# Performance work log

Hardware: AMD Instinct MI355X
Metric: run time of the kernel (lower is better)

Reference implementation:

```python
import jax, jax.numpy as jnp
import numpy as np

FP8_MAX = 448.0  # torch.finfo(float8_e4m3fn).max


def per_tensor_quantize(t):
    amax = jnp.max(jnp.abs(t))
    scale = jnp.maximum(amax, 1e-12) / FP8_MAX
    q = jnp.clip(t / scale, -FP8_MAX, FP8_MAX)
    return q, scale.astype(jnp.float32)


def fp8_cast(t):
    # round-to-fp8-e4m3 and back (value-faithful to .to(float8_e4m3fn)),
    # straight-through so it is also usable under vjp
    rounded = t.astype(jnp.float8_e4m3fn).astype(t.dtype)
    return t + jax.lax.stop_gradient(rounded - t)


def setup_inputs() -> dict:
    key = jax.random.key(0)
    k1, k2, k3 = jax.random.split(key, 3)
    B, S, D_IN, D_OUT = 4, 2048, 4096, 4096
    x = jax.random.normal(k1, (B, S, D_IN), dtype=jnp.float32)
    # build a pre-quantized weight exactly like the repo would: quantize a float weight
    w = jax.random.normal(k2, (D_OUT, D_IN), dtype=jnp.float32) * 0.02
    qweight, weight_scale = per_tensor_quantize(w)
    bias = jax.random.normal(k3, (D_OUT,), dtype=jnp.float32) * 0.01
    return {"x": x, "qweight": qweight, "weight_scale": weight_scale, "bias": bias}


def reference(x, qweight, weight_scale, bias):
    quantize_output = True  # init kwarg
    # quantize activation per-tensor
    qinput, input_scale = per_tensor_quantize(x)
    qinput = fp8_cast(qinput)          # .to(float8_e4m3fn)
    qw = fp8_cast(qweight)             # .to(qdtype)
    # dequant-scaled GEMM: linear(A*sa, B*sb) + bias
    a = qinput * input_scale.astype(x.dtype)
    b = qw * weight_scale.astype(x.dtype)
    out = jnp.einsum('bsd,od->bso', a, b) + bias
    if quantize_output:
        qout, out_scale = per_tensor_quantize(out)  # clamp only, no fp8 cast (matches torch)
        out = qout * out_scale
    return out
```

## Files before the change

### kernel.cpp

```cpp
#include <hip/hip_runtime.h>
#include <stdint.h>

#define FP8_MAX 448.0f

typedef float f32x16 __attribute__((ext_vector_type(16)));
typedef int i32x8 __attribute__((ext_vector_type(8)));


__device__ __forceinline__ void async_load16(const void* gptr, void* lptr) {
  __builtin_amdgcn_global_load_lds(
      (const __attribute__((address_space(1))) unsigned int*)(uintptr_t)gptr,
      (__attribute__((address_space(3))) unsigned int*)(unsigned)(uintptr_t)lptr,
      16, 0, 0);
}

__device__ __forceinline__ unsigned pack4_fp8(float a, float b, float c, float d) {
  int v = __builtin_amdgcn_cvt_pk_fp8_f32(a, b, 0, false);
  v = __builtin_amdgcn_cvt_pk_fp8_f32(c, d, v, true);
  return (unsigned)v;
}

__device__ __forceinline__ float clip_fp8(float q) {
  return fminf(FP8_MAX, fmaxf(-FP8_MAX, q));
}

__device__ __forceinline__ i32x8 frag32(const unsigned char* rowbase, int o_lo, int o_hi) {
  uint4 lo = *(const uint4*)(rowbase + o_lo);
  uint4 hi = *(const uint4*)(rowbase + o_hi);
  i32x8 f;
  f[0] = lo.x; f[1] = lo.y; f[2] = lo.z; f[3] = lo.w;
  f[4] = hi.x; f[5] = hi.y; f[6] = hi.z; f[7] = hi.w;
  return f;
}


__global__ void k_amax(const float4* __restrict__ x, long n4, unsigned* __restrict__ out) {
  float m = 0.f;
  const long stride = (long)gridDim.x * blockDim.x;
  for (long i = (long)blockIdx.x * blockDim.x + threadIdx.x; i < n4; i += stride) {
    float4 v = x[i];
    m = fmaxf(m, fmaxf(fmaxf(fabsf(v.x), fabsf(v.y)), fmaxf(fabsf(v.z), fabsf(v.w))));
  }
#pragma unroll
  for (int off = 32; off > 0; off >>= 1)
    m = fmaxf(m, __shfl_xor(m, off, 64));
  __shared__ float sm[4];
  const int wv = threadIdx.x >> 6;
  if ((threadIdx.x & 63) == 0) sm[wv] = m;
  __syncthreads();
  if (threadIdx.x == 0) {
    m = fmaxf(fmaxf(sm[0], sm[1]), fmaxf(sm[2], sm[3]));
    atomicMax(out, __float_as_uint(m));
  }
}


__global__ void k_quant_x(const float4* __restrict__ x, unsigned* __restrict__ q,
                          const unsigned* __restrict__ amax_bits) {
  const float scale = fmaxf(__uint_as_float(*amax_bits), 1e-12f) / 448.0f;
  const long i0 = (long)blockIdx.x * blockDim.x + threadIdx.x;
  const long stride = (long)gridDim.x * blockDim.x;
#pragma unroll
  for (int r = 0; r < 4; r++) {
    const long i = i0 + r * stride;
    float4 v = x[i];
    q[i] = pack4_fp8(clip_fp8(v.x / scale), clip_fp8(v.y / scale),
                     clip_fp8(v.z / scale), clip_fp8(v.w / scale));
  }
}


__global__ void k_quant_w(const float4* __restrict__ w, unsigned* __restrict__ q) {
  const long i0 = (long)blockIdx.x * blockDim.x + threadIdx.x;
  const long stride = (long)gridDim.x * blockDim.x;
#pragma unroll
  for (int r = 0; r < 4; r++) {
    const long i = i0 + r * stride;
    float4 v = w[i];
    q[i] = pack4_fp8(clip_fp8(v.x), clip_fp8(v.y), clip_fp8(v.z), clip_fp8(v.w));
  }
}


__global__ __launch_bounds__(256, 2) void k_gemm(
    const unsigned char* __restrict__ qa, const unsigned char* __restrict__ qb,
    const unsigned* __restrict__ amax_bits, const float* __restrict__ wscale,
    const float* __restrict__ bias, float* __restrict__ out,
    int M, int N, int K) {
  __shared__ unsigned char lds_a[128 * 64];
  __shared__ unsigned char lds_b[256 * 64];

  const int t = threadIdx.x;
  const int lane = t & 63;
  const int wv = t >> 6;
  const int wm = wv >> 1, wn = wv & 1;
  const int lr = lane & 31;
  const int h = lane >> 5;

  const int bx = blockIdx.x;
  const int by = blockIdx.y;

  const unsigned char* Ag = qa + (size_t)by * 128 * K;
  const unsigned char* Bg = qb + (size_t)bx * 256 * K;

  size_t a_goff[2]; int a_doff[2];
#pragma unroll
  for (int r = 0; r < 2; r++) {
    const int idx = t + r * 256;
    const int row = idx >> 2;
    const int ch = (idx & 3) ^ ((row >> 1) & 3);
    a_goff[r] = (size_t)row * K + (size_t)ch * 16;
    a_doff[r] = idx * 16;
  }
  size_t b_goff[4]; int b_doff[4];
#pragma unroll
  for (int r = 0; r < 4; r++) {
    const int idx = t + r * 256;
    const int row = idx >> 2;
    const int ch = (idx & 3) ^ ((row >> 1) & 3);
    b_goff[r] = (size_t)row * K + (size_t)ch * 16;
    b_doff[r] = idx * 16;
  }

  const int g = (lr >> 1) & 3;
  const int c_lo = ((2 * h + 0) ^ g) * 16;
  const int c_hi = ((2 * h + 1) ^ g) * 16;
  int arow[2], brow[4];
#pragma unroll
  for (int i = 0; i < 2; i++) arow[i] = (wm * 64 + i * 32 + lr) * 64;
#pragma unroll
  for (int j = 0; j < 4; j++) brow[j] = (wn * 128 + j * 32 + lr) * 64;

  f32x16 acc[2][4];
#pragma unroll
  for (int i = 0; i < 2; i++)
#pragma unroll
    for (int j = 0; j < 4; j++)
#pragma unroll
      for (int r = 0; r < 16; r++) acc[i][j][r] = 0.f;

  for (int kt = 0; kt < K; kt += 64) {
#pragma unroll
    for (int r = 0; r < 2; r++) async_load16(Ag + a_goff[r] + kt, lds_a + a_doff[r]);
#pragma unroll
    for (int r = 0; r < 4; r++) async_load16(Bg + b_goff[r] + kt, lds_b + b_doff[r]);
    __syncthreads();

    i32x8 af[2], bf[4];
#pragma unroll
    for (int i = 0; i < 2; i++) af[i] = frag32(lds_a + arow[i], c_lo, c_hi);
#pragma unroll
    for (int j = 0; j < 4; j++) bf[j] = frag32(lds_b + brow[j], c_lo, c_hi);

#pragma unroll
    for (int i = 0; i < 2; i++)
#pragma unroll
      for (int j = 0; j < 4; j++)
        acc[i][j] = __builtin_amdgcn_mfma_scale_f32_32x32x64_f8f6f4(
            af[i], bf[j], acc[i][j], 0, 0, 0, 0x7f7f7f7f, 0, 0x7f7f7f7f);
    __syncthreads();
  }

  const float s_comb =
      (fmaxf(__uint_as_float(*amax_bits), 1e-12f) / 448.0f) * wscale[0];
  const int m_base = by * 128 + wm * 64;
  const int n_base = bx * 256 + wn * 128;
#pragma unroll
  for (int j = 0; j < 4; j++) {
    const int col = n_base + j * 32 + lr;
    const float bv = bias[col];
#pragma unroll
    for (int i = 0; i < 2; i++) {
      const int row0 = m_base + i * 32 + 4 * h;
#pragma unroll
      for (int r = 0; r < 16; r++) {
        const int row = row0 + (r & 3) + 8 * (r >> 2);
        out[(size_t)row * N + col] = acc[i][j][r] * s_comb + bv;
      }
    }
  }
}


extern "C" void kernel_launch(void* const* d_in, const int* in_sizes, int n_in,
                              void* d_out, int out_size, void* d_ws, size_t ws_size,
                              hipStream_t stream) {
  const float* x = (const float*)d_in[0];
  const float* qw = (const float*)d_in[1];
  const float* wscale = (const float*)d_in[2];
  const float* bias = (const float*)d_in[3];

  const int N = in_sizes[3];
  const int K = in_sizes[1] / N;
  const int M = in_sizes[0] / K;

  const long nx = (long)M * K;
  const long nw = (long)N * K;

  unsigned char* ws = (unsigned char*)d_ws;
  unsigned* amax_bits = (unsigned*)ws;
  unsigned char* qx8 = ws + 256;
  unsigned char* qw8 = qx8 + nx;

  float* out = (float*)d_out;

  hipMemsetAsync(d_ws, 0, 4, stream);
  k_amax<<<2048, 256, 0, stream>>>((const float4*)x, nx / 4, amax_bits);
  k_quant_x<<<(int)(nx / 4 / 4 / 256), 256, 0, stream>>>(
      (const float4*)x, (unsigned*)qx8, amax_bits);
  k_quant_w<<<(int)(nw / 4 / 4 / 256), 256, 0, stream>>>(
      (const float4*)qw, (unsigned*)qw8);
  dim3 grid(N / 256, M / 128);
  k_gemm<<<grid, 256, 0, stream>>>(qx8, qw8, amax_bits, wscale, bias, out, M, N, K);
}
```

Measured before the change: 449.7 us.

## Rework FP8 GEMM into 256x256 double-buffered tiles with XCD-aware block remap

```diff
diff --git a/kernel.cpp b/kernel.cpp
--- a/kernel.cpp
+++ b/kernel.cpp
@@ -82,100 +82,144 @@
 }
 
 
-__global__ __launch_bounds__(256, 2) void k_gemm(
+__global__ __launch_bounds__(512, 2) void k_gemm(
     const unsigned char* __restrict__ qa, const unsigned char* __restrict__ qb,
     const unsigned* __restrict__ amax_bits, const float* __restrict__ wscale,
     const float* __restrict__ bias, float* __restrict__ out,
     int M, int N, int K) {
-  __shared__ unsigned char lds_a[128 * 64];
-  __shared__ unsigned char lds_b[256 * 64];
+  __shared__ unsigned char lds[131072];
 
   const int t = threadIdx.x;
   const int lane = t & 63;
   const int wv = t >> 6;
-  const int wm = wv >> 1, wn = wv & 1;
+  const int wm = wv >> 2;
+  const int wn = wv & 3;
   const int lr = lane & 31;
   const int h = lane >> 5;
-
-  const int bx = blockIdx.x;
-  const int by = blockIdx.y;
-
-  const unsigned char* Ag = qa + (size_t)by * 128 * K;
+  const int g = lr & 7;
+
+  const int nwg = gridDim.x;
+  int wg = blockIdx.x;
+  if ((nwg & 7) == 0) wg = (wg & 7) * (nwg >> 3) + (wg >> 3);
+  const int nby = M >> 8;
+  const int bx = wg / nby;
+  const int by = wg - bx * nby;
+
+  const unsigned char* Ag = qa + (size_t)by * 256 * K;
   const unsigned char* Bg = qb + (size_t)bx * 256 * K;
 
-  size_t a_goff[2]; int a_doff[2];
+  size_t gsw[2]; int ldso[2];
 #pragma unroll
   for (int r = 0; r < 2; r++) {
-    const int idx = t + r * 256;
-    const int row = idx >> 2;
-    const int ch = (idx & 3) ^ ((row >> 1) & 3);
-    a_goff[r] = (size_t)row * K + (size_t)ch * 16;
-    a_doff[r] = idx * 16;
-  }
-  size_t b_goff[4]; int b_doff[4];
-#pragma unroll
-  for (int r = 0; r < 4; r++) {
-    const int idx = t + r * 256;
-    const int row = idx >> 2;
-    const int ch = (idx & 3) ^ ((row >> 1) & 3);
-    b_goff[r] = (size_t)row * K + (size_t)ch * 16;
-    b_doff[r] = idx * 16;
-  }
-
-  const int g = (lr >> 1) & 3;
-  const int c_lo = ((2 * h + 0) ^ g) * 16;
-  const int c_hi = ((2 * h + 1) ^ g) * 16;
-  int arow[2], brow[4];
-#pragma unroll
-  for (int i = 0; i < 2; i++) arow[i] = (wm * 64 + i * 32 + lr) * 64;
-#pragma unroll
-  for (int j = 0; j < 4; j++) brow[j] = (wn * 128 + j * 32 + lr) * 64;
-
-  f32x16 acc[2][4];
-#pragma unroll
-  for (int i = 0; i < 2; i++)
-#pragma unroll
-    for (int j = 0; j < 4; j++)
+    const int idx = t + r * 512;
+    const int row = idx >> 3;
+    const int cs = idx & 7;
+    gsw[r] = (size_t)row * K + (size_t)((cs ^ (row & 7)) << 4);
+    ldso[r] = idx << 4;
+  }
+
+  const int cb[2] = { ((2 * h) ^ g) << 4, (((2 * h) | 4) ^ g) << 4 };
+  const int a_base = (wm * 128 + lr) * 128;
+  const int b_base = (wn * 64 + lr) * 128;
+
+  f32x16 acc[4][2];
+#pragma unroll
+  for (int i = 0; i < 4; i++)
+#pragma unroll
+    for (int j = 0; j < 2; j++)
 #pragma unroll
       for (int r = 0; r < 16; r++) acc[i][j][r] = 0.f;
 
-  for (int kt = 0; kt < K; kt += 64) {
-#pragma unroll
-    for (int r = 0; r < 2; r++) async_load16(Ag + a_goff[r] + kt, lds_a + a_doff[r]);
-#pragma unroll
-    for (int r = 0; r < 4; r++) async_load16(Bg + b_goff[r] + kt, lds_b + b_doff[r]);
-    __syncthreads();
-
-    i32x8 af[2], bf[4];
-#pragma unroll
-    for (int i = 0; i < 2; i++) af[i] = frag32(lds_a + arow[i], c_lo, c_hi);
-#pragma unroll
-    for (int j = 0; j < 4; j++) bf[j] = frag32(lds_b + brow[j], c_lo, c_hi);
-
-#pragma unroll
-    for (int i = 0; i < 2; i++)
-#pragma unroll
-      for (int j = 0; j < 4; j++)
-        acc[i][j] = __builtin_amdgcn_mfma_scale_f32_32x32x64_f8f6f4(
-            af[i], bf[j], acc[i][j], 0, 0, 0, 0x7f7f7f7f, 0, 0x7f7f7f7f);
-    __syncthreads();
+#pragma unroll
+  for (int u = 0; u < 2; u++)
+#pragma unroll
+    for (int r = 0; r < 2; r++) {
+      async_load16(Ag + (size_t)u * 128 * K + gsw[r], lds + u * 16384 + ldso[r]);
+      async_load16(Bg + (size_t)u * 128 * K + gsw[r], lds + 65536 + u * 16384 + ldso[r]);
+    }
+  asm volatile("s_waitcnt vmcnt(0)" ::: "memory");
+  __builtin_amdgcn_s_barrier();
+
+  const int NT = K >> 7;
+  int buf = 0;
+  for (int tile = 0; tile < NT; ++tile) {
+    const unsigned char* ldsA = lds + buf * 32768;
+    const unsigned char* ldsB = lds + 65536 + buf * 32768;
+    unsigned char* stA = lds + (buf ^ 1) * 32768;
+    unsigned char* stB = lds + 65536 + (buf ^ 1) * 32768;
+    const bool have_next = (tile + 1 < NT);
+    const size_t kb_next = (size_t)(tile + 1) << 7;
+
+#pragma unroll
+    for (int q = 0; q < 4; ++q) {
+      const int mp = q >> 1, nj = q & 1;
+
+      i32x8 af[2][2], bf[2];
+#pragma unroll
+      for (int im = 0; im < 2; ++im) {
+        const unsigned char* rb = ldsA + a_base + (2 * mp + im) * 4096;
+#pragma unroll
+        for (int kk = 0; kk < 2; ++kk)
+          af[im][kk] = frag32(rb, cb[kk], cb[kk] ^ 16);
+      }
+      {
+        const unsigned char* rb = ldsB + b_base + nj * 4096;
+#pragma unroll
+        for (int kk = 0; kk < 2; ++kk)
+          bf[kk] = frag32(rb, cb[kk], cb[kk] ^ 16);
+      }
+
+      if (q == 0 && have_next) {
+#pragma unroll
+        for (int u = 0; u < 2; u++)
+#pragma unroll
+          for (int r = 0; r < 2; r++)
+            async_load16(Ag + (size_t)u * 128 * K + gsw[r] + kb_next,
+                         stA + u * 16384 + ldso[r]);
+      }
+      if (q == 1 && have_next) {
+#pragma unroll
+        for (int u = 0; u < 2; u++)
+#pragma unroll
+          for (int r = 0; r < 2; r++)
+            async_load16(Bg + (size_t)u * 128 * K + gsw[r] + kb_next,
+                         stB + u * 16384 + ldso[r]);
+      }
+
+      __builtin_amdgcn_s_barrier();
+      asm volatile("s_waitcnt lgkmcnt(0)" ::: "memory");
+      __builtin_amdgcn_sched_barrier(0);
+      __builtin_amdgcn_s_setprio(1);
+#pragma unroll
+      for (int kk = 0; kk < 2; ++kk)
+#pragma unroll
+        for (int im = 0; im < 2; ++im)
+          acc[2 * mp + im][nj] = __builtin_amdgcn_mfma_scale_f32_32x32x64_f8f6f4(
+              af[im][kk], bf[kk], acc[2 * mp + im][nj], 0, 0, 0,
+              0x7f7f7f7f, 0, 0x7f7f7f7f);
+      __builtin_amdgcn_s_setprio(0);
+      __builtin_amdgcn_sched_barrier(0);
+      __builtin_amdgcn_s_barrier();
+    }
+
+    asm volatile("s_waitcnt vmcnt(0)" ::: "memory");
+    __builtin_amdgcn_s_barrier();
+    buf ^= 1;
   }
 
   const float s_comb =
       (fmaxf(__uint_as_float(*amax_bits), 1e-12f) / 448.0f) * wscale[0];
-  const int m_base = by * 128 + wm * 64;
-  const int n_base = bx * 256 + wn * 128;
-#pragma unroll
-  for (int j = 0; j < 4; j++) {
-    const int col = n_base + j * 32 + lr;
+#pragma unroll
+  for (int nj = 0; nj < 2; ++nj) {
+    const int col = bx * 256 + wn * 64 + nj * 32 + lr;
     const float bv = bias[col];
 #pragma unroll
-    for (int i = 0; i < 2; i++) {
-      const int row0 = m_base + i * 32 + 4 * h;
-#pragma unroll
-      for (int r = 0; r < 16; r++) {
+    for (int mi = 0; mi < 4; ++mi) {
+      const int row0 = by * 256 + wm * 128 + mi * 32 + 4 * h;
+#pragma unroll
+      for (int r = 0; r < 16; ++r) {
         const int row = row0 + (r & 3) + 8 * (r >> 2);
-        out[(size_t)row * N + col] = acc[i][j][r] * s_comb + bv;
+        out[(size_t)row * N + col] = acc[mi][nj][r] * s_comb + bv;
       }
     }
   }
@@ -210,6 +254,7 @@
       (const float4*)x, (unsigned*)qx8, amax_bits);
   k_quant_w<<<(int)(nw / 4 / 4 / 256), 256, 0, stream>>>(
       (const float4*)qw, (unsigned*)qw8);
-  dim3 grid(N / 256, M / 128);
-  k_gemm<<<grid, 256, 0, stream>>>(qx8, qw8, amax_bits, wscale, bias, out, M, N, K);
-}
+  const int nwg = (N / 256) * (M / 256);
+  k_gemm<<<dim3(nwg), 512, 0, stream>>>(qx8, qw8, amax_bits, wscale, bias, out,
+                                        M, N, K);
+}
```

Measured after the change: 569.1 us. 26.5% more time.
